# Optimization experiments

Measured on AMD Instinct MI355X. Metric: run time of the kernel, lower is better.

## Reference

```python
import jax, jax.numpy as jnp
import numpy as np

N, E, G = 30000, 60000, 1200
EMB, HID, OUT = 768, 384, 768
NEG = 0.01  # leaky_relu negative slope (torch default / GATConv negative_slope)


def _seg_softmax(a, idx, num):
    m = jax.ops.segment_max(a, idx, num_segments=num)
    e = jnp.exp(a - m[idx])
    s = jax.ops.segment_sum(e, idx, num_segments=num)
    return e / (s[idx] + 1e-16)


def _gru(x, h, Wi, Wh, bi, bh):
    gi = x @ Wi + bi
    gh = h @ Wh + bh
    ir, iz, in_ = jnp.split(gi, 3, -1)
    hr, hz, hn = jnp.split(gh, 3, -1)
    r = jax.nn.sigmoid(ir + hr)
    z = jax.nn.sigmoid(iz + hz)
    n = jnp.tanh(in_ + r * hn)
    return (1.0 - z) * n + z * h


def setup_inputs() -> dict:
    key = jax.random.key(0)
    ks = iter(jax.random.split(key, 64))
    def W(*shape):
        return jax.random.normal(next(ks), shape, jnp.float32) / np.sqrt(shape[0])
    z = lambda *s: jnp.zeros(s, jnp.float32)
    inp = {}
    inp['x_idx'] = jax.random.randint(next(ks), (N, 9), 0, 178)
    inp['edge_index'] = jax.random.randint(next(ks), (2, E), 0, N)
    inp['edge_attr_idx'] = jax.random.randint(next(ks), (E, 3), 0, 18)
    inp['batch'] = jnp.sort(jax.random.randint(next(ks), (N,), 0, G))
    inp['x_emb'] = W(178, EMB)
    inp['e_emb'] = W(18, EMB)
    inp['lin1_W'] = W(EMB, HID); inp['lin1_b'] = z(HID)
    inp['att_l'] = W(HID); inp['att_r'] = W(HID)
    inp['gl1_W'] = W(HID + EMB, HID); inp['gl2_W'] = W(HID, HID); inp['gate_b'] = z(HID)
    inp['gru1_Wi'] = W(HID, 3 * HID); inp['gru1_Wh'] = W(HID, 3 * HID)
    inp['gru1_bi'] = z(3 * HID); inp['gru1_bh'] = z(3 * HID)
    inp['gat_W'] = W(HID, HID); inp['gat_as'] = W(HID); inp['gat_ad'] = W(HID); inp['gat_b'] = z(HID)
    inp['gru2_Wi'] = W(HID, 3 * HID); inp['gru2_Wh'] = W(HID, 3 * HID)
    inp['gru2_bi'] = z(3 * HID); inp['gru2_bh'] = z(3 * HID)
    inp['mol_W'] = W(HID, HID); inp['mol_as'] = W(HID); inp['mol_ad'] = W(HID); inp['mol_b'] = z(HID)
    inp['mgru_Wi'] = W(HID, 3 * HID); inp['mgru_Wh'] = W(HID, 3 * HID)
    inp['mgru_bi'] = z(3 * HID); inp['mgru_bh'] = z(3 * HID)
    inp['lin2_W'] = W(HID, OUT); inp['lin2_b'] = z(OUT)
    return inp


def reference(x_idx, edge_index, edge_attr_idx, batch,
              x_emb, e_emb, lin1_W, lin1_b,
              att_l, att_r, gl1_W, gl2_W, gate_b,
              gru1_Wi, gru1_Wh, gru1_bi, gru1_bh,
              gat_W, gat_as, gat_ad, gat_b,
              gru2_Wi, gru2_Wh, gru2_bi, gru2_bh,
              mol_W, mol_as, mol_ad, mol_b,
              mgru_Wi, mgru_Wh, mgru_bi, mgru_bh,
              lin2_W, lin2_b):
    src, dst = edge_index[0], edge_index[1]
    # embedding-sum over feature columns
    x = x_emb[x_idx].sum(1)            # [N, EMB]
    ea = e_emb[edge_attr_idx].sum(1)   # [E, EMB]
    x = jax.nn.leaky_relu(x @ lin1_W + lin1_b, NEG)  # [N, HID]
    # --- GATEConv (edge-attr attention) ---
    m = jax.nn.leaky_relu(jnp.concatenate([x[src], ea], -1) @ gl1_W, NEG)  # [E, HID]
    a = jax.nn.leaky_relu(m @ att_l + x[dst] @ att_r, NEG)
    a = _seg_softmax(a, dst, N)
    h = jax.ops.segment_sum((m @ gl2_W) * a[:, None], dst, num_segments=N) + gate_b
    x = jax.nn.relu(_gru(jax.nn.elu(h), x, gru1_Wi, gru1_Wh, gru1_bi, gru1_bh))
    # --- atom GATConv (num_layers=2 -> one extra layer, heads=1, no self-loops) ---
    xl = x @ gat_W
    a = jax.nn.leaky_relu((xl @ gat_as)[src] + (xl @ gat_ad)[dst], NEG)
    a = _seg_softmax(a, dst, N)
    h = jax.ops.segment_sum(xl[src] * a[:, None], dst, num_segments=N) + gat_b
    x = jax.nn.relu(_gru(jax.nn.elu(h), x, gru2_Wi, gru2_Wh, gru2_bi, gru2_bh))
    # --- attentive molecule readout, num_timesteps=3 ---
    out = jax.nn.relu(jax.ops.segment_sum(x, batch, num_segments=G))  # [G, HID]
    xl = x @ mol_W
    a_node = xl @ mol_as  # per-node source attention term (fixed across timesteps)
    for _ in range(3):
        a_g = (out @ mol_W) @ mol_ad
        a = jax.nn.leaky_relu(a_node + a_g[batch], NEG)
        a = _seg_softmax(a, batch, G)
        h = jax.ops.segment_sum(xl * a[:, None], batch, num_segments=G) + mol_b
        out = jax.nn.relu(_gru(jax.nn.elu(h), out, mgru_Wi, mgru_Wh, mgru_bi, mgru_bh))
    return out @ lin2_W + lin2_b  # [G, OUT]
```

## Files before the change

### kernel.cpp

```cpp
#include <hip/hip_runtime.h>
#include <cstdint>
#include <cstddef>

#define NN 30000
#define NE 60000
#define NG 1200
#define HID 384
#define EMB 768
#define OUTD 768
#define NEGS 0.01f

typedef _Float16 f16;
typedef _Float16 f16x8 __attribute__((ext_vector_type(8)));
typedef float f32x16 __attribute__((ext_vector_type(16)));

static __device__ __forceinline__ float leaky(float x){ return x > 0.f ? x : NEGS * x; }
static __device__ __forceinline__ float elu1(float x){ return x > 0.f ? x : (expf(x) - 1.f); }
static __device__ __forceinline__ float sigm(float x){ return 1.f / (1.f + expf(-x)); }

static __device__ __forceinline__ void atomicMaxF(float* a, float v){
  if (v >= 0.f) atomicMax((int*)a, __float_as_int(v));
  else atomicMin((unsigned int*)a, __float_as_uint(v));
}

static __device__ __forceinline__ size_t pf_idx(int row, int col){
  return (((((size_t)(row >> 5)) * 24 + (col >> 4)) * 2 + ((col >> 3) & 1)) * 32
          + (row & 31)) * 8 + (col & 7);
}
#define PF_RB_STRIDE 12288
#define PF_KS_STRIDE 512
#define PF_GATE_STRIDE 147456

__global__ __launch_bounds__(256) void k_gemm(
    const float* __restrict__ A, const float* __restrict__ B,
    const float* __restrict__ bias, float* __restrict__ C,
    int M, int N, int K, int act)
{
  __shared__ float As[16][65];
  __shared__ float Bs[16][65];
  const int tid = threadIdx.x;
  const int tx = tid & 15, ty = tid >> 4;
  const int row0 = blockIdx.y * 64, col0 = blockIdx.x * 64;
  const int ar = tid >> 2, ak = (tid & 3) << 2;
  const int bk = tid >> 4, bc = (tid & 15) << 2;
  float acc[4][4] = {};
  for (int k0 = 0; k0 < K; k0 += 16) {
    float4 av = make_float4(0.f, 0.f, 0.f, 0.f);
    if (row0 + ar < M)
      av = *(const float4*)(A + (size_t)(row0 + ar) * K + k0 + ak);
    As[ak + 0][ar] = av.x; As[ak + 1][ar] = av.y;
    As[ak + 2][ar] = av.z; As[ak + 3][ar] = av.w;
    float4 bv = *(const float4*)(B + (size_t)(k0 + bk) * N + col0 + bc);
    Bs[bk][bc + 0] = bv.x; Bs[bk][bc + 1] = bv.y;
    Bs[bk][bc + 2] = bv.z; Bs[bk][bc + 3] = bv.w;
    __syncthreads();
#pragma unroll
    for (int kk = 0; kk < 16; kk++) {
      float a[4], b[4];
#pragma unroll
      for (int i = 0; i < 4; i++) a[i] = As[kk][(ty << 2) + i];
#pragma unroll
      for (int j = 0; j < 4; j++) b[j] = Bs[kk][(tx << 2) + j];
#pragma unroll
      for (int i = 0; i < 4; i++)
#pragma unroll
        for (int j = 0; j < 4; j++)
          acc[i][j] = fmaf(a[i], b[j], acc[i][j]);
    }
    __syncthreads();
  }
#pragma unroll
  for (int i = 0; i < 4; i++) {
    int r = row0 + (ty << 2) + i;
    if (r >= M) continue;
#pragma unroll
    for (int j = 0; j < 4; j++) {
      int c = col0 + (tx << 2) + j;
      float v = acc[i][j];
      if (bias) v += bias[c];
      if (act == 1) v = leaky(v);
      else if (act == 2) v = elu1(v);
      else if (act == 3) v = fmaxf(v, 0.f);
      C[(size_t)r * N + c] = v;
    }
  }
}

__global__ __launch_bounds__(256) void k_hgemm(
    const f16* __restrict__ Apf, const f16* __restrict__ Bpf,
    const float* __restrict__ bias, float* __restrict__ Cf, f16* __restrict__ Ch,
    int M, int Nn, int act)
{
  const int nct = Nn >> 7;
  const int id = blockIdx.x;
  const int lane8 = id & 7, chunk = id >> 3;
  const int ct = chunk % nct, rg = chunk / nct;
  const int rt = rg * 8 + lane8;
  const int Mt = (M + 127) >> 7;
  if (rt >= Mt) return;
  const int r0 = rt * 128, n0 = ct * 128;
  const int tid = threadIdx.x;
  const int wid = tid >> 6, lane = tid & 63;
  const int wr = wid >> 1, wc = wid & 1;
  const int l31 = lane & 31, lhi = lane >> 5;
  const size_t lane_off = (size_t)(lhi * 32 + l31) * 8;
  const f16* pA[2]; const f16* pB[2];
#pragma unroll
  for (int i = 0; i < 2; i++) {
    pA[i] = Apf + (size_t)(r0 / 32 + wr * 2 + i) * PF_RB_STRIDE + lane_off;
    pB[i] = Bpf + (size_t)(n0 / 32 + wc * 2 + i) * PF_RB_STRIDE + lane_off;
  }
  f32x16 acc[2][2];
#pragma unroll
  for (int i = 0; i < 2; i++)
#pragma unroll
    for (int j = 0; j < 2; j++)
#pragma unroll
      for (int r = 0; r < 16; r++) acc[i][j][r] = 0.f;
  f16x8 af[2], bf[2], naf[2], nbf[2];
#pragma unroll
  for (int i = 0; i < 2; i++) { af[i] = *(const f16x8*)(pA[i]); bf[i] = *(const f16x8*)(pB[i]); }
#pragma unroll 4
  for (int ks = 0; ks < 24; ks++) {
    const size_t noff = (size_t)(ks < 23 ? ks + 1 : 23) * PF_KS_STRIDE;
#pragma unroll
    for (int i = 0; i < 2; i++) { naf[i] = *(const f16x8*)(pA[i] + noff); nbf[i] = *(const f16x8*)(pB[i] + noff); }
#pragma unroll
    for (int i = 0; i < 2; i++)
#pragma unroll
      for (int j = 0; j < 2; j++)
        acc[i][j] = __builtin_amdgcn_mfma_f32_32x32x16_f16(af[i], bf[j], acc[i][j], 0, 0, 0);
#pragma unroll
    for (int i = 0; i < 2; i++) { af[i] = naf[i]; bf[i] = nbf[i]; }
  }
#pragma unroll
  for (int i = 0; i < 2; i++)
#pragma unroll
    for (int j = 0; j < 2; j++) {
      int col = n0 + wc * 64 + j * 32 + l31;
      float bv = bias ? bias[col] : 0.f;
#pragma unroll
      for (int r = 0; r < 16; r++) {
        int row = r0 + wr * 64 + i * 32 + (r & 3) + 8 * (r >> 2) + 4 * lhi;
        if (row < M) {
          float v = acc[i][j][r] + bv;
          if (act == 1) v = leaky(v);
          else if (act == 2) v = elu1(v);
          else if (act == 3) v = fmaxf(v, 0.f);
          if (Cf) Cf[(size_t)row * Nn + col] = v;
          if (Ch) Ch[pf_idx(row, col)] = (f16)v;
        }
      }
    }
}

__global__ __launch_bounds__(256) void k_gru_hgemm(
    const f16* __restrict__ Upf, const f16* __restrict__ Hpf,
    const f16* __restrict__ Wip, const f16* __restrict__ Whp,
    const float* __restrict__ bi, const float* __restrict__ bh,
    float* __restrict__ Xo, f16* __restrict__ Xoh, int M)
{
  const int id = blockIdx.x;
  const int lane8 = id & 7, chunk = id >> 3;
  const int ct = chunk % 6, rg = chunk / 6;
  const int rt = rg * 8 + lane8;
  const int Mt = (M + 63) >> 6;
  if (rt >= Mt) return;
  const int r0 = rt * 64, c0 = ct * 64;
  const int tid = threadIdx.x;
  const int wid = tid >> 6, lane = tid & 63;
  const int wr = wid >> 1, wc = wid & 1;
  const int l31 = lane & 31, lhi = lane >> 5;
  const size_t lane_off = (size_t)(lhi * 32 + l31) * 8;
  const f16* pU  = Upf + (size_t)(r0 / 32 + wr) * PF_RB_STRIDE + lane_off;
  const f16* pH  = Hpf + (size_t)(r0 / 32 + wr) * PF_RB_STRIDE + lane_off;
  const f16* pWi = Wip + (size_t)(c0 / 32 + wc) * PF_RB_STRIDE + lane_off;
  const f16* pWh = Whp + (size_t)(c0 / 32 + wc) * PF_RB_STRIDE + lane_off;
#define Z16 {0,0,0,0,0,0,0,0,0,0,0,0,0,0,0,0}
  f32x16 accR = Z16, accZ = Z16, aN = Z16, hN = Z16;
  f16x8 au, ah, bir, biz, bin, bhr, bhz, bhn;
  f16x8 nau, nah, nbir, nbiz, nbin, nbhr, nbhz, nbhn;
  au  = *(const f16x8*)(pU);
  ah  = *(const f16x8*)(pH);
  bir = *(const f16x8*)(pWi);
  biz = *(const f16x8*)(pWi + PF_GATE_STRIDE);
  bin = *(const f16x8*)(pWi + 2 * PF_GATE_STRIDE);
  bhr = *(const f16x8*)(pWh);
  bhz = *(const f16x8*)(pWh + PF_GATE_STRIDE);
  bhn = *(const f16x8*)(pWh + 2 * PF_GATE_STRIDE);
#pragma unroll 4
  for (int ks = 0; ks < 24; ks++) {
    const size_t noff = (size_t)(ks < 23 ? ks + 1 : 23) * PF_KS_STRIDE;
    nau  = *(const f16x8*)(pU + noff);
    nah  = *(const f16x8*)(pH + noff);
    nbir = *(const f16x8*)(pWi + noff);
    nbiz = *(const f16x8*)(pWi + PF_GATE_STRIDE + noff);
    nbin = *(const f16x8*)(pWi + 2 * PF_GATE_STRIDE + noff);
    nbhr = *(const f16x8*)(pWh + noff);
    nbhz = *(const f16x8*)(pWh + PF_GATE_STRIDE + noff);
    nbhn = *(const f16x8*)(pWh + 2 * PF_GATE_STRIDE + noff);
    accR = __builtin_amdgcn_mfma_f32_32x32x16_f16(au, bir, accR, 0, 0, 0);
    accR = __builtin_amdgcn_mfma_f32_32x32x16_f16(ah, bhr, accR, 0, 0, 0);
    accZ = __builtin_amdgcn_mfma_f32_32x32x16_f16(au, biz, accZ, 0, 0, 0);
    accZ = __builtin_amdgcn_mfma_f32_32x32x16_f16(ah, bhz, accZ, 0, 0, 0);
    aN   = __builtin_amdgcn_mfma_f32_32x32x16_f16(au, bin, aN, 0, 0, 0);
    hN   = __builtin_amdgcn_mfma_f32_32x32x16_f16(ah, bhn, hN, 0, 0, 0);
    au = nau; ah = nah; bir = nbir; biz = nbiz; bin = nbin;
    bhr = nbhr; bhz = nbhz; bhn = nbhn;
  }
  const int col = c0 + wc * 32 + l31;
  const float brz = bi[col] + bh[col];
  const float bzz = bi[HID + col] + bh[HID + col];
  const float bin_ = bi[2 * HID + col];
  const float bhn_ = bh[2 * HID + col];
#pragma unroll
  for (int r = 0; r < 16; r++) {
    int row = r0 + wr * 32 + (r & 3) + 8 * (r >> 2) + 4 * lhi;
    if (row < M) {
      float rg_ = sigm(accR[r] + brz);
      float zg  = sigm(accZ[r] + bzz);
      float ng  = tanhf(aN[r] + bin_ + rg_ * (hN[r] + bhn_));
      float hp  = (float)Hpf[pf_idx(row, col)];
      float o = (1.f - zg) * ng + zg * hp;
      o = fmaxf(o, 0.f);
      if (Xo) Xo[(size_t)row * HID + col] = o;
      Xoh[pf_idx(row, col)] = (f16)o;
    }
  }
}

__global__ void k_wpack_all(
    const float* __restrict__ w0, const float* __restrict__ w1,
    const float* __restrict__ w2, const float* __restrict__ w3,
    const float* __restrict__ w4, const float* __restrict__ w5,
    const float* __restrict__ w6, const float* __restrict__ w7,
    const float* __restrict__ w8, const float* __restrict__ w9,
    const float* __restrict__ w10,
    f16* __restrict__ d0, f16* __restrict__ d1, f16* __restrict__ d2,
    f16* __restrict__ d3, f16* __restrict__ d4, f16* __restrict__ d5,
    f16* __restrict__ d6, f16* __restrict__ d7, f16* __restrict__ d8,
    f16* __restrict__ d9, f16* __restrict__ d10)
{
  long t = (long)blockIdx.x * blockDim.x + threadIdx.x;
  if (t >= 3538944L) return;
  const float* W; f16* Wp; int Nn; long tt;
  if (t < 589824L) {
    int s = (int)(t / 147456L); tt = t - (long)s * 147456L; Nn = HID;
    if (s == 0) { W = w0; Wp = d0; } else if (s == 1) { W = w1; Wp = d1; }
    else if (s == 2) { W = w2; Wp = d2; } else { W = w3; Wp = d3; }
  } else if (t < 3244032L) {
    long u = t - 589824L;
    int s = (int)(u / 442368L); tt = u - (long)s * 442368L; Nn = 3 * HID;
    if (s == 0) { W = w4; Wp = d4; } else if (s == 1) { W = w5; Wp = d5; }
    else if (s == 2) { W = w6; Wp = d6; } else if (s == 3) { W = w7; Wp = d7; }
    else if (s == 4) { W = w8; Wp = d8; } else { W = w9; Wp = d9; }
  } else {
    tt = t - 3244032L; Nn = OUTD; W = w10; Wp = d10;
  }
  int elem = (int)(tt & 7); long c = tt >> 3;
  int l31 = (int)(c & 31); long q = c >> 5;
  int lhi = (int)(q & 1); long p = q >> 1;
  int ks = (int)(p % 24); int rb = (int)(p / 24);
  int n = rb * 32 + l31, k = ks * 16 + lhi * 8 + elem;
  Wp[tt] = (f16)W[(size_t)k * Nn + n];
}

__global__ void k_f2h_pf(const float* __restrict__ in, f16* __restrict__ out, long total)
{
  long t = (long)blockIdx.x * blockDim.x + threadIdx.x;
  if (t >= total) return;
  int i = (int)(t / HID), c = (int)(t % HID);
  out[pf_idx(i, c)] = (f16)in[t];
}

__global__ void k_node_embed2(const int* __restrict__ xi, const float* __restrict__ T1,
                              const float* __restrict__ b, const float* __restrict__ att_r,
                              f16* __restrict__ x1h, float* __restrict__ xr, int n)
{
  int w = (int)(((long)blockIdx.x * blockDim.x + threadIdx.x) >> 6);
  int lane = threadIdx.x & 63;
  if (w >= n) return;
  int idx[9];
#pragma unroll
  for (int j = 0; j < 9; j++) idx[j] = xi[w * 9 + j];
  float s = 0.f;
#pragma unroll
  for (int t = 0; t < 6; t++) {
    int c = lane + 64 * t;
    float v = b[c];
#pragma unroll
    for (int j = 0; j < 9; j++) v += T1[(size_t)idx[j] * HID + c];
    v = leaky(v);
    x1h[pf_idx(w, c)] = (f16)v;
    s += v * att_r[c];
  }
  for (int o = 32; o; o >>= 1) s += __shfl_down(s, o, 64);
  if (lane == 0) xr[w] = s;
}

__global__ void k_rowdot(const float* __restrict__ X, const float* __restrict__ v,
                         float* __restrict__ out, int M)
{
  int w = (int)(((long)blockIdx.x * blockDim.x + threadIdx.x) >> 6);
  int lane = threadIdx.x & 63;
  if (w >= M) return;
  float s = 0.f;
  for (int j = lane; j < HID; j += 64) s += X[(size_t)w * HID + j] * v[j];
  for (int o = 32; o; o >>= 1) s += __shfl_down(s, o, 64);
  if (lane == 0) out[w] = s;
}

__global__ void k_rowdot2(const float* __restrict__ X, const float* __restrict__ v1,
                          const float* __restrict__ v2, float* __restrict__ o1,
                          float* __restrict__ o2, int M)
{
  int w = (int)(((long)blockIdx.x * blockDim.x + threadIdx.x) >> 6);
  int lane = threadIdx.x & 63;
  if (w >= M) return;
  float s1 = 0.f, s2 = 0.f;
  for (int j = lane; j < HID; j += 64) {
    float x = X[(size_t)w * HID + j];
    s1 += x * v1[j]; s2 += x * v2[j];
  }
  for (int o = 32; o; o >>= 1) { s1 += __shfl_down(s1, o, 64); s2 += __shfl_down(s2, o, 64); }
  if (lane == 0) { o1[w] = s1; o2[w] = s2; }
}

__global__ void k_init_ms(float* __restrict__ mx, float* __restrict__ sum, int n)
{
  int t = (int)((long)blockIdx.x * blockDim.x + threadIdx.x);
  if (t >= n) return;
  mx[t] = __int_as_float(0xFF800000);
  sum[t] = 0.f;
}

__global__ void k_gbounds(const int* __restrict__ batch, int* __restrict__ gstart, int n, int G)
{
  int g = (int)((long)blockIdx.x * blockDim.x + threadIdx.x);
  if (g > G) return;
  int lo = 0, hi = n;
  while (lo < hi) { int mid = (lo + hi) >> 1; if (batch[mid] < g) lo = mid + 1; else hi = mid; }
  gstart[g] = lo;
}

__global__ __launch_bounds__(384) void k_mol_iter(
    const float* __restrict__ cur, const float* __restrict__ XLm,
    const float* __restrict__ a_node, const float* __restrict__ w_g,
    const float* __restrict__ mol_b, const int* __restrict__ gstart,
    f16* __restrict__ HMp)
{
  const int g = blockIdx.x;
  const int tid = threadIdx.x;
  const int lane = tid & 63, wv = tid >> 6;
  __shared__ float red[6];
  __shared__ float wbuf[384];
  __shared__ float sh[3];
  const int s0 = gstart[g], s1 = gstart[g + 1];
  float p = cur[(size_t)g * HID + tid] * w_g[tid];
  for (int o = 32; o; o >>= 1) p += __shfl_down(p, o, 64);
  if (lane == 0) red[wv] = p;
  __syncthreads();
  if (tid == 0) { float s = 0.f; for (int i = 0; i < 6; i++) s += red[i]; sh[0] = s; }
  __syncthreads();
  const float ag = sh[0];
  float mx = -3.4e38f;
  for (int n = s0 + tid; n < s1; n += 384) mx = fmaxf(mx, leaky(a_node[n] + ag));
  for (int o = 32; o; o >>= 1) mx = fmaxf(mx, __shfl_down(mx, o, 64));
  __syncthreads();
  if (lane == 0) red[wv] = mx;
  __syncthreads();
  if (tid == 0) { float m = red[0]; for (int i = 1; i < 6; i++) m = fmaxf(m, red[i]); sh[1] = m; }
  __syncthreads();
  const float gmx = sh[1];
  float sm = 0.f;
  for (int n = s0 + tid; n < s1; n += 384) sm += expf(leaky(a_node[n] + ag) - gmx);
  for (int o = 32; o; o >>= 1) sm += __shfl_down(sm, o, 64);
  __syncthreads();
  if (lane == 0) red[wv] = sm;
  __syncthreads();
  if (tid == 0) { float s = 0.f; for (int i = 0; i < 6; i++) s += red[i]; sh[2] = s; }
  __syncthreads();
  const float inv = 1.f / (sh[2] + 1e-16f);
  float h = 0.f;
  for (int base = s0; base < s1; base += 384) {
    int cnt = min(384, s1 - base);
    __syncthreads();
    if (tid < cnt) wbuf[tid] = expf(leaky(a_node[base + tid] + ag) - gmx) * inv;
    __syncthreads();
    for (int k = 0; k < cnt; k++) h += XLm[(size_t)(base + k) * HID + tid] * wbuf[k];
  }
  h = elu1(h + mol_b[tid]);
  HMp[pf_idx(g, tid)] = (f16)h;
}

__global__ void k_gate_att(const float* __restrict__ P, const float* __restrict__ Te,
                           const int* __restrict__ ei, const int* __restrict__ eai,
                           const float* __restrict__ attl, const float* __restrict__ xr,
                           float* __restrict__ aE, float* __restrict__ mx, int ne)
{
  int e = (int)(((long)blockIdx.x * blockDim.x + threadIdx.x) >> 6);
  int lane = threadIdx.x & 63;
  if (e >= ne) return;
  int s = ei[e];
  int i0 = eai[e * 3], i1 = eai[e * 3 + 1], i2 = eai[e * 3 + 2];
  float acc = 0.f;
  for (int j = lane; j < HID; j += 64) {
    float m = P[(size_t)s * HID + j] + Te[(size_t)i0 * HID + j]
            + Te[(size_t)i1 * HID + j] + Te[(size_t)i2 * HID + j];
    acc += leaky(m) * attl[j];
  }
  for (int o = 32; o; o >>= 1) acc += __shfl_down(acc, o, 64);
  if (lane == 0) {
    int d = ei[NE + e];
    float a = leaky(acc + xr[d]);
    aE[e] = a;
    atomicMaxF(&mx[d], a);
  }
}

__global__ void k_gat_att(const float* __restrict__ sS, const float* __restrict__ sD,
                          const int* __restrict__ ei, float* __restrict__ aE,
                          float* __restrict__ mx, int ne)
{
  int e = (int)((long)blockIdx.x * blockDim.x + threadIdx.x);
  if (e >= ne) return;
  int s = ei[e], d = ei[NE + e];
  float a = leaky(sS[s] + sD[d]);
  aE[e] = a;
  atomicMaxF(&mx[d], a);
}

__global__ void k_seg_exp(float* __restrict__ a, const int* __restrict__ idx,
                          const float* __restrict__ mx, float* __restrict__ sum, int n)
{
  int t = (int)((long)blockIdx.x * blockDim.x + threadIdx.x);
  if (t >= n) return;
  int d = idx[t];
  float e = expf(a[t] - mx[d]);
  a[t] = e;
  atomicAdd(&sum[d], e);
}

__global__ void k_scatter_edge(const float* __restrict__ P, const float* __restrict__ Te,
                               const int* __restrict__ ei, const int* __restrict__ eai,
                               const float* __restrict__ aE, const float* __restrict__ sum,
                               float* __restrict__ acc, long total)
{
  long t = (long)blockIdx.x * blockDim.x + threadIdx.x;
  if (t >= total) return;
  int e = (int)(t / HID), c = (int)(t % HID);
  int s = ei[e], d = ei[NE + e];
  float m = P[(size_t)s * HID + c] + Te[(size_t)eai[e * 3] * HID + c]
          + Te[(size_t)eai[e * 3 + 1] * HID + c] + Te[(size_t)eai[e * 3 + 2] * HID + c];
  m = leaky(m);
  float w = aE[e] / (sum[d] + 1e-16f);
  atomicAdd(&acc[(size_t)d * HID + c], m * w);
}

__global__ void k_scatter_gat(const float* __restrict__ XL, const float* __restrict__ aE,
                              const float* __restrict__ sum, const int* __restrict__ ei,
                              float* __restrict__ acc, long total)
{
  long t = (long)blockIdx.x * blockDim.x + threadIdx.x;
  if (t >= total) return;
  int e = (int)(t / HID), c = (int)(t % HID);
  int s = ei[e], d = ei[NE + e];
  float w = aE[e] / (sum[d] + 1e-16f);
  atomicAdd(&acc[(size_t)d * HID + c], XL[(size_t)s * HID + c] * w);
}

__global__ void k_scatter_sum_pf(const f16* __restrict__ Xpf, const int* __restrict__ batch,
                                 float* __restrict__ acc, long total)
{
  long t = (long)blockIdx.x * blockDim.x + threadIdx.x;
  if (t >= total) return;
  int i = (int)(t / HID), c = (int)(t % HID);
  atomicAdd(&acc[(size_t)batch[i] * HID + c], (float)Xpf[pf_idx(i, c)]);
}

__global__ void k_bias_act(float* __restrict__ X, const float* __restrict__ bias,
                           f16* __restrict__ Xh, long total, int act)
{
  long t = (long)blockIdx.x * blockDim.x + threadIdx.x;
  if (t >= total) return;
  int i = (int)(t / HID), c = (int)(t % HID);
  float v = X[t];
  if (bias) v += bias[c];
  if (act == 2) v = elu1(v);
  else if (act == 3) v = fmaxf(v, 0.f);
  X[t] = v;
  if (Xh) Xh[pf_idx(i, c)] = (f16)v;
}

extern "C" void kernel_launch(void* const* d_in, const int* in_sizes, int n_in,
                              void* d_out, int out_size, void* d_ws, size_t ws_size,
                              hipStream_t stream)
{
  const int* x_idx = (const int*)d_in[0];
  const int* edge_index = (const int*)d_in[1];
  const int* eai = (const int*)d_in[2];
  const int* batch = (const int*)d_in[3];
  const float* x_emb = (const float*)d_in[4];
  const float* e_emb = (const float*)d_in[5];
  const float* lin1_W = (const float*)d_in[6];
  const float* lin1_b = (const float*)d_in[7];
  const float* att_l = (const float*)d_in[8];
  const float* att_r = (const float*)d_in[9];
  const float* gl1_W = (const float*)d_in[10];
  const float* gl2_W = (const float*)d_in[11];
  const float* gate_b = (const float*)d_in[12];
  const float* gru1_Wi = (const float*)d_in[13];
  const float* gru1_Wh = (const float*)d_in[14];
  const float* gru1_bi = (const float*)d_in[15];
  const float* gru1_bh = (const float*)d_in[16];
  const float* gat_W = (const float*)d_in[17];
  const float* gat_as = (const float*)d_in[18];
  const float* gat_ad = (const float*)d_in[19];
  const float* gat_b = (const float*)d_in[20];
  const float* gru2_Wi = (const float*)d_in[21];
  const float* gru2_Wh = (const float*)d_in[22];
  const float* gru2_bi = (const float*)d_in[23];
  const float* gru2_bh = (const float*)d_in[24];
  const float* mol_W = (const float*)d_in[25];
  const float* mol_as = (const float*)d_in[26];
  const float* mol_ad = (const float*)d_in[27];
  const float* mol_b = (const float*)d_in[28];
  const float* mgru_Wi = (const float*)d_in[29];
  const float* mgru_Wh = (const float*)d_in[30];
  const float* mgru_bi = (const float*)d_in[31];
  const float* mgru_bh = (const float*)d_in[32];
  const float* lin2_W = (const float*)d_in[33];
  const float* lin2_b = (const float*)d_in[34];
  float* outp = (float*)d_out;

  const size_t NB = (size_t)NN * HID;
  const size_t GB = (size_t)NG * HID;
  const size_t PFH = (size_t)940 * PF_RB_STRIDE;
  const size_t PFG = (size_t)40 * PF_RB_STRIDE;

  float* ws = (float*)d_ws;
  size_t off = 0;
  auto alloc = [&](size_t n) { float* p = ws + off; off += n; return p; };
  auto alloch = [&](size_t n) { f16* p = (f16*)(ws + off); off += (n + 1) / 2; return p; };
  float* A    = alloc(NB);
  float* B    = alloc(NB);
  float* C    = alloc(NB);
  f16* H1 = alloch(PFH);
  f16* H2 = alloch(PFH);
  f16* H3 = alloch(PFH);
  f16* W1p   = alloch((size_t)HID * HID);
  f16* W2p   = alloch((size_t)HID * HID);
  f16* Wgatp = alloch((size_t)HID * HID);
  f16* Wmolp = alloch((size_t)HID * HID);
  f16* Wg1ip = alloch((size_t)3 * HID * HID);
  f16* Wg1hp = alloch((size_t)3 * HID * HID);
  f16* Wg2ip = alloch((size_t)3 * HID * HID);
  f16* Wg2hp = alloch((size_t)3 * HID * HID);
  f16* Wmgip = alloch((size_t)3 * HID * HID);
  f16* Wmghp = alloch((size_t)3 * HID * HID);
  f16* Wl2p  = alloch((size_t)HID * OUTD);
  f16* OUTaPF = alloch(PFG);
  f16* OUTbPF = alloch(PFG);
  f16* HMp    = alloch(PFG);
  float* T1   = alloc((size_t)178 * HID);
  float* Te   = alloc((size_t)18 * HID);
  float* w_g  = alloc(HID);
  float* xr   = alloc(NN);
  float* sS   = alloc(NN);
  float* sD   = alloc(NN);
  float* mxN  = alloc(NN);
  float* sumN = alloc(NN);
  float* a_node = alloc(NN);
  float* aE   = alloc(NE);
  float* OUTa = alloc(GB);
  float* OUTb = alloc(GB);
  int* gstart = (int*)alloc(NG + 1);
  (void)n_in; (void)in_sizes; (void)out_size;
  if (ws_size < off * sizeof(float)) return;

  const int* dstArr = edge_index + NE;
  dim3 blk(256);
  auto g1 = [](long n) { return dim3((unsigned)((n + 255) / 256)); };
  auto gw = [](long waves) { return dim3((unsigned)((waves * 64 + 255) / 256)); };
  const long NBt = (long)NB, EBt = (long)NE * HID, GBt = (long)GB;
  const int MtH = (NN + 127) / 128;
  const dim3 gH((unsigned)(8 * 3 * ((MtH + 7) / 8)));
  const int MtR = (NN + 63) / 64;
  const dim3 gR((unsigned)(8 * 6 * ((MtR + 7) / 8)));
  const int MtGH = (NG + 127) / 128;
  const dim3 gF((unsigned)(8 * 6 * ((MtGH + 7) / 8)));
  const int MtGR = (NG + 63) / 64;
  const dim3 gRG((unsigned)(8 * 6 * ((MtGR + 7) / 8)));

  hipLaunchKernelGGL(k_wpack_all, g1(3538944L), blk, 0, stream,
                     gl1_W, gl2_W, gat_W, mol_W,
                     gru1_Wi, gru1_Wh, gru2_Wi, gru2_Wh, mgru_Wi, mgru_Wh, lin2_W,
                     W1p, W2p, Wgatp, Wmolp,
                     Wg1ip, Wg1hp, Wg2ip, Wg2hp, Wmgip, Wmghp, Wl2p);

  hipLaunchKernelGGL(k_gemm, dim3(HID / 64, 3), blk, 0, stream,
                     x_emb, lin1_W, nullptr, T1, 178, HID, EMB, 0);
  hipLaunchKernelGGL(k_gemm, dim3(HID / 64, 1), blk, 0, stream,
                     e_emb, gl1_W + (size_t)HID * HID, nullptr, Te, 18, HID, EMB, 0);
  hipLaunchKernelGGL(k_rowdot, gw(HID), blk, 0, stream, mol_W, mol_ad, w_g, HID);
  hipLaunchKernelGGL(k_gbounds, g1(NG + 1), blk, 0, stream, batch, gstart, NN, NG);

  hipLaunchKernelGGL(k_node_embed2, gw(NN), blk, 0, stream, x_idx, T1, lin1_b, att_r, H1, xr, NN);

  hipLaunchKernelGGL(k_hgemm, gH, blk, 0, stream, H1, W1p, nullptr, B, (f16*)nullptr, NN, HID, 0);
  hipLaunchKernelGGL(k_init_ms, g1(NN), blk, 0, stream, mxN, sumN, NN);
  hipLaunchKernelGGL(k_gate_att, gw(NE), blk, 0, stream, B, Te, edge_index, eai, att_l, xr, aE, mxN, NE);
  hipLaunchKernelGGL(k_seg_exp, g1(NE), blk, 0, stream, aE, dstArr, mxN, sumN, NE);
  hipMemsetAsync(C, 0, NB * sizeof(float), stream);
  hipLaunchKernelGGL(k_scatter_edge, g1(EBt), blk, 0, stream, B, Te, edge_index, eai, aE, sumN, C, EBt);
  hipLaunchKernelGGL(k_f2h_pf, g1(NBt), blk, 0, stream, C, H2, NBt);
  hipLaunchKernelGGL(k_hgemm, gH, blk, 0, stream, H2, W2p, gate_b, (float*)nullptr, H3, NN, HID, 2);
  hipLaunchKernelGGL(k_gru_hgemm, gR, blk, 0, stream, H3, H1, Wg1ip, Wg1hp,
                     gru1_bi, gru1_bh, (float*)nullptr, H2, NN);

  hipLaunchKernelGGL(k_hgemm, gH, blk, 0, stream, H2, Wgatp, nullptr, B, (f16*)nullptr, NN, HID, 0);
  hipLaunchKernelGGL(k_rowdot2, gw(NN), blk, 0, stream, B, gat_as, gat_ad, sS, sD, NN);
  hipLaunchKernelGGL(k_init_ms, g1(NN), blk, 0, stream, mxN, sumN, NN);
  hipLaunchKernelGGL(k_gat_att, g1(NE), blk, 0, stream, sS, sD, edge_index, aE, mxN, NE);
  hipLaunchKernelGGL(k_seg_exp, g1(NE), blk, 0, stream, aE, dstArr, mxN, sumN, NE);
  hipMemsetAsync(A, 0, NB * sizeof(float), stream);
  hipLaunchKernelGGL(k_scatter_gat, g1(EBt), blk, 0, stream, B, aE, sumN, edge_index, A, EBt);
  hipLaunchKernelGGL(k_bias_act, g1(NBt), blk, 0, stream, A, gat_b, H1, NBt, 2);
  hipLaunchKernelGGL(k_gru_hgemm, gR, blk, 0, stream, H1, H2, Wg2ip, Wg2hp,
                     gru2_bi, gru2_bh, (float*)nullptr, H3, NN);

  hipMemsetAsync(OUTa, 0, GB * sizeof(float), stream);
  hipLaunchKernelGGL(k_scatter_sum_pf, g1(NBt), blk, 0, stream, H3, batch, OUTa, NBt);
  hipLaunchKernelGGL(k_bias_act, g1(GBt), blk, 0, stream, OUTa, (const float*)nullptr, OUTaPF, GBt, 3);
  hipLaunchKernelGGL(k_hgemm, gH, blk, 0, stream, H3, Wmolp, nullptr, A, (f16*)nullptr, NN, HID, 0);
  hipLaunchKernelGGL(k_rowdot, gw(NN), blk, 0, stream, A, mol_as, a_node, NN);

  float* cur = OUTa;   f16* curPF = OUTaPF;
  float* nxt = OUTb;   f16* nxtPF = OUTbPF;
  for (int t = 0; t < 3; t++) {
    hipLaunchKernelGGL(k_mol_iter, dim3(NG), dim3(384), 0, stream,
                       cur, A, a_node, w_g, mol_b, gstart, HMp);
    hipLaunchKernelGGL(k_gru_hgemm, gRG, blk, 0, stream, HMp, curPF, Wmgip, Wmghp,
                       mgru_bi, mgru_bh, nxt, nxtPF, NG);
    float* tf = cur; cur = nxt; nxt = tf;
    f16* th = curPF; curPF = nxtPF; nxtPF = th;
  }

  hipLaunchKernelGGL(k_hgemm, gF, blk, 0, stream, curPF, Wl2p, lin2_b, outp, (f16*)nullptr, NG, OUTD, 0);
}
```

Baseline: 964.2 us.

## Replace atomic edge scatter with CSR-by-destination online-softmax gather aggregation

Builds a CSR edge list grouped by destination (degree count, single-block scan, fill) and replaces the separate attention, segment max, exp-sum and per-element atomic scatter kernels with one wave per node that computes an online softmax and accumulates messages in registers. The GAT layer gets the same treatment, fusing bias and ELU into the f16 packed output. The molecule sum switches from atomic scatter to a contiguous per-graph reduction over the fp32 GRU output. This removes large float atomic traffic, several memsets and conversion passes, at the cost of CSR-build kernels and possible imbalance on high-degree nodes.

Measured after the change: 795.2 us. -17.5%, faster.

```diff
diff --git a/kernel.cpp b/kernel.cpp
--- a/kernel.cpp
+++ b/kernel.cpp
@@ -17,11 +17,6 @@
 static __device__ __forceinline__ float leaky(float x){ return x > 0.f ? x : NEGS * x; }
 static __device__ __forceinline__ float elu1(float x){ return x > 0.f ? x : (expf(x) - 1.f); }
 static __device__ __forceinline__ float sigm(float x){ return 1.f / (1.f + expf(-x)); }
-
-static __device__ __forceinline__ void atomicMaxF(float* a, float v){
-  if (v >= 0.f) atomicMax((int*)a, __float_as_int(v));
-  else atomicMin((unsigned int*)a, __float_as_uint(v));
-}
 
 static __device__ __forceinline__ size_t pf_idx(int row, int col){
   return (((((size_t)(row >> 5)) * 24 + (col >> 4)) * 2 + ((col >> 3) & 1)) * 32
@@ -265,14 +260,6 @@
   Wp[tt] = (f16)W[(size_t)k * Nn + n];
 }
 
-__global__ void k_f2h_pf(const float* __restrict__ in, f16* __restrict__ out, long total)
-{
-  long t = (long)blockIdx.x * blockDim.x + threadIdx.x;
-  if (t >= total) return;
-  int i = (int)(t / HID), c = (int)(t % HID);
-  out[pf_idx(i, c)] = (f16)in[t];
-}
-
 __global__ void k_node_embed2(const int* __restrict__ xi, const float* __restrict__ T1,
                               const float* __restrict__ b, const float* __restrict__ att_r,
                               f16* __restrict__ x1h, float* __restrict__ xr, int n)
@@ -326,14 +313,6 @@
   if (lane == 0) { o1[w] = s1; o2[w] = s2; }
 }
 
-__global__ void k_init_ms(float* __restrict__ mx, float* __restrict__ sum, int n)
-{
-  int t = (int)((long)blockIdx.x * blockDim.x + threadIdx.x);
-  if (t >= n) return;
-  mx[t] = __int_as_float(0xFF800000);
-  sum[t] = 0.f;
-}
-
 __global__ void k_gbounds(const int* __restrict__ batch, int* __restrict__ gstart, int n, int G)
 {
   int g = (int)((long)blockIdx.x * blockDim.x + threadIdx.x);
@@ -341,6 +320,150 @@
   int lo = 0, hi = n;
   while (lo < hi) { int mid = (lo + hi) >> 1; if (batch[mid] < g) lo = mid + 1; else hi = mid; }
   gstart[g] = lo;
+}
+
+__global__ void k_deg(const int* __restrict__ dst, int* __restrict__ cnt, int ne)
+{
+  int e = (int)((long)blockIdx.x * blockDim.x + threadIdx.x);
+  if (e >= ne) return;
+  atomicAdd(&cnt[dst[e]], 1);
+}
+
+__global__ __launch_bounds__(1024) void k_scan(const int* __restrict__ cnt,
+                                               int* __restrict__ rowptr,
+                                               int* __restrict__ cursor)
+{
+  __shared__ int part[1024];
+  const int tid = threadIdx.x;
+  const int c0 = tid * 30, c1 = min(c0 + 30, NN);
+  int s = 0;
+  for (int i = c0; i < c1; i++) s += cnt[i];
+  part[tid] = s;
+  __syncthreads();
+  for (int o = 1; o < 1024; o <<= 1) {
+    int v = (tid >= o) ? part[tid - o] : 0;
+    __syncthreads();
+    part[tid] += v;
+    __syncthreads();
+  }
+  int run = (tid ? part[tid - 1] : 0);
+  for (int i = c0; i < c1; i++) { rowptr[i] = run; cursor[i] = run; run += cnt[i]; }
+  if (tid == 1023) rowptr[NN] = part[1023];
+}
+
+__global__ void k_fill(const int* __restrict__ dst, int* __restrict__ cursor,
+                       int* __restrict__ elist, int ne)
+{
+  int e = (int)((long)blockIdx.x * blockDim.x + threadIdx.x);
+  if (e >= ne) return;
+  int p = atomicAdd(&cursor[dst[e]], 1);
+  elist[p] = e;
+}
+
+__global__ void k_gate_agg(const float* __restrict__ P, const float* __restrict__ Te,
+                           const int* __restrict__ ei, const int* __restrict__ eai,
+                           const float* __restrict__ attl, const float* __restrict__ xr,
+                           const int* __restrict__ rowptr, const int* __restrict__ elist,
+                           f16* __restrict__ Hout, int n)
+{
+  int node = (int)(((long)blockIdx.x * blockDim.x + threadIdx.x) >> 6);
+  int lane = threadIdx.x & 63;
+  if (node >= n) return;
+  const int e0 = rowptr[node], e1 = rowptr[node + 1];
+  const float xrd = xr[node];
+  float h0 = 0.f, h1 = 0.f, h2 = 0.f, h3 = 0.f, h4 = 0.f, h5 = 0.f;
+  float mx = -3.4e38f, s = 0.f;
+  for (int q = e0; q < e1; q++) {
+    int e = elist[q];
+    int src = ei[e];
+    int i0 = eai[e * 3], i1 = eai[e * 3 + 1], i2 = eai[e * 3 + 2];
+    float m[6];
+    float dot = 0.f;
+#pragma unroll
+    for (int t = 0; t < 6; t++) {
+      int c = lane + 64 * t;
+      float v = P[(size_t)src * HID + c] + Te[(size_t)i0 * HID + c]
+              + Te[(size_t)i1 * HID + c] + Te[(size_t)i2 * HID + c];
+      v = leaky(v);
+      m[t] = v;
+      dot += v * attl[c];
+    }
+#pragma unroll
+    for (int o = 32; o; o >>= 1) dot += __shfl_xor(dot, o, 64);
+    float a = leaky(dot + xrd);
+    if (a > mx) {
+      float f = expf(mx - a);
+      s *= f; h0 *= f; h1 *= f; h2 *= f; h3 *= f; h4 *= f; h5 *= f;
+      mx = a;
+    }
+    float w = expf(a - mx);
+    s += w;
+    h0 += w * m[0]; h1 += w * m[1]; h2 += w * m[2];
+    h3 += w * m[3]; h4 += w * m[4]; h5 += w * m[5];
+  }
+  const float inv = 1.f / (s + 1e-16f);
+  Hout[pf_idx(node, lane)]           = (f16)(h0 * inv);
+  Hout[pf_idx(node, lane + 64)]      = (f16)(h1 * inv);
+  Hout[pf_idx(node, lane + 128)]     = (f16)(h2 * inv);
+  Hout[pf_idx(node, lane + 192)]     = (f16)(h3 * inv);
+  Hout[pf_idx(node, lane + 256)]     = (f16)(h4 * inv);
+  Hout[pf_idx(node, lane + 320)]     = (f16)(h5 * inv);
+}
+
+__global__ void k_gat_agg(const float* __restrict__ XL, const int* __restrict__ ei,
+                          const float* __restrict__ sS, const float* __restrict__ sD,
+                          const float* __restrict__ gat_b,
+                          const int* __restrict__ rowptr, const int* __restrict__ elist,
+                          f16* __restrict__ Hout, int n)
+{
+  int node = (int)(((long)blockIdx.x * blockDim.x + threadIdx.x) >> 6);
+  int lane = threadIdx.x & 63;
+  if (node >= n) return;
+  const int e0 = rowptr[node], e1 = rowptr[node + 1];
+  const float sDn = sD[node];
+  float h0 = 0.f, h1 = 0.f, h2 = 0.f, h3 = 0.f, h4 = 0.f, h5 = 0.f;
+  float mx = -3.4e38f, s = 0.f;
+  for (int q = e0; q < e1; q++) {
+    int e = elist[q];
+    int src = ei[e];
+    float a = leaky(sS[src] + sDn);
+    if (a > mx) {
+      float f = expf(mx - a);
+      s *= f; h0 *= f; h1 *= f; h2 *= f; h3 *= f; h4 *= f; h5 *= f;
+      mx = a;
+    }
+    float w = expf(a - mx);
+    s += w;
+    const float* row = XL + (size_t)src * HID;
+    h0 += w * row[lane];
+    h1 += w * row[lane + 64];
+    h2 += w * row[lane + 128];
+    h3 += w * row[lane + 192];
+    h4 += w * row[lane + 256];
+    h5 += w * row[lane + 320];
+  }
+  const float inv = 1.f / (s + 1e-16f);
+  Hout[pf_idx(node, lane)]       = (f16)elu1(h0 * inv + gat_b[lane]);
+  Hout[pf_idx(node, lane + 64)]  = (f16)elu1(h1 * inv + gat_b[lane + 64]);
+  Hout[pf_idx(node, lane + 128)] = (f16)elu1(h2 * inv + gat_b[lane + 128]);
+  Hout[pf_idx(node, lane + 192)] = (f16)elu1(h3 * inv + gat_b[lane + 192]);
+  Hout[pf_idx(node, lane + 256)] = (f16)elu1(h4 * inv + gat_b[lane + 256]);
+  Hout[pf_idx(node, lane + 320)] = (f16)elu1(h5 * inv + gat_b[lane + 320]);
+}
+
+__global__ __launch_bounds__(384) void k_graph_sum(const float* __restrict__ X,
+                                                   const int* __restrict__ gstart,
+                                                   float* __restrict__ OUTa,
+                                                   f16* __restrict__ OUTaPF)
+{
+  const int g = blockIdx.x;
+  const int tid = threadIdx.x;
+  const int s0 = gstart[g], s1 = gstart[g + 1];
+  float acc = 0.f;
+  for (int i = s0; i < s1; i++) acc += X[(size_t)i * HID + tid];
+  acc = fmaxf(acc, 0.f);
+  OUTa[(size_t)g * HID + tid] = acc;
+  OUTaPF[pf_idx(g, tid)] = (f16)acc;
 }
 
 __global__ __launch_bounds__(384) void k_mol_iter(
@@ -391,105 +514,6 @@
   }
   h = elu1(h + mol_b[tid]);
   HMp[pf_idx(g, tid)] = (f16)h;
-}
-
-__global__ void k_gate_att(const float* __restrict__ P, const float* __restrict__ Te,
-                           const int* __restrict__ ei, const int* __restrict__ eai,
-                           const float* __restrict__ attl, const float* __restrict__ xr,
-                           float* __restrict__ aE, float* __restrict__ mx, int ne)
-{
-  int e = (int)(((long)blockIdx.x * blockDim.x + threadIdx.x) >> 6);
-  int lane = threadIdx.x & 63;
-  if (e >= ne) return;
-  int s = ei[e];
-  int i0 = eai[e * 3], i1 = eai[e * 3 + 1], i2 = eai[e * 3 + 2];
-  float acc = 0.f;
-  for (int j = lane; j < HID; j += 64) {
-    float m = P[(size_t)s * HID + j] + Te[(size_t)i0 * HID + j]
-            + Te[(size_t)i1 * HID + j] + Te[(size_t)i2 * HID + j];
-    acc += leaky(m) * attl[j];
-  }
-  for (int o = 32; o; o >>= 1) acc += __shfl_down(acc, o, 64);
-  if (lane == 0) {
-    int d = ei[NE + e];
-    float a = leaky(acc + xr[d]);
-    aE[e] = a;
-    atomicMaxF(&mx[d], a);
-  }
-}
-
-__global__ void k_gat_att(const float* __restrict__ sS, const float* __restrict__ sD,
-                          const int* __restrict__ ei, float* __restrict__ aE,
-                          float* __restrict__ mx, int ne)
-{
-  int e = (int)((long)blockIdx.x * blockDim.x + threadIdx.x);
-  if (e >= ne) return;
-  int s = ei[e], d = ei[NE + e];
-  float a = leaky(sS[s] + sD[d]);
-  aE[e] = a;
-  atomicMaxF(&mx[d], a);
-}
-
-__global__ void k_seg_exp(float* __restrict__ a, const int* __restrict__ idx,
-                          const float* __restrict__ mx, float* __restrict__ sum, int n)
-{
-  int t = (int)((long)blockIdx.x * blockDim.x + threadIdx.x);
-  if (t >= n) return;
-  int d = idx[t];
-  float e = expf(a[t] - mx[d]);
-  a[t] = e;
-  atomicAdd(&sum[d], e);
-}
-
-__global__ void k_scatter_edge(const float* __restrict__ P, const float* __restrict__ Te,
-                               const int* __restrict__ ei, const int* __restrict__ eai,
-                               const float* __restrict__ aE, const float* __restrict__ sum,
-                               float* __restrict__ acc, long total)
-{
-  long t = (long)blockIdx.x * blockDim.x + threadIdx.x;
-  if (t >= total) return;
-  int e = (int)(t / HID), c = (int)(t % HID);
-  int s = ei[e], d = ei[NE + e];
-  float m = P[(size_t)s * HID + c] + Te[(size_t)eai[e * 3] * HID + c]
-          + Te[(size_t)eai[e * 3 + 1] * HID + c] + Te[(size_t)eai[e * 3 + 2] * HID + c];
-  m = leaky(m);
-  float w = aE[e] / (sum[d] + 1e-16f);
-  atomicAdd(&acc[(size_t)d * HID + c], m * w);
-}
-
-__global__ void k_scatter_gat(const float* __restrict__ XL, const float* __restrict__ aE,
-                              const float* __restrict__ sum, const int* __restrict__ ei,
-                              float* __restrict__ acc, long total)
-{
-  long t = (long)blockIdx.x * blockDim.x + threadIdx.x;
-  if (t >= total) return;
-  int e = (int)(t / HID), c = (int)(t % HID);
-  int s = ei[e], d = ei[NE + e];
-  float w = aE[e] / (sum[d] + 1e-16f);
-  atomicAdd(&acc[(size_t)d * HID + c], XL[(size_t)s * HID + c] * w);
-}
-
-__global__ void k_scatter_sum_pf(const f16* __restrict__ Xpf, const int* __restrict__ batch,
-                                 float* __restrict__ acc, long total)
-{
-  long t = (long)blockIdx.x * blockDim.x + threadIdx.x;
-  if (t >= total) return;
-  int i = (int)(t / HID), c = (int)(t % HID);
-  atomicAdd(&acc[(size_t)batch[i] * HID + c], (float)Xpf[pf_idx(i, c)]);
-}
-
-__global__ void k_bias_act(float* __restrict__ X, const float* __restrict__ bias,
-                           f16* __restrict__ Xh, long total, int act)
-{
-  long t = (long)blockIdx.x * blockDim.x + threadIdx.x;
-  if (t >= total) return;
-  int i = (int)(t / HID), c = (int)(t % HID);
-  float v = X[t];
-  if (bias) v += bias[c];
-  if (act == 2) v = elu1(v);
-  else if (act == 3) v = fmaxf(v, 0.f);
-  X[t] = v;
-  if (Xh) Xh[pf_idx(i, c)] = (f16)v;
 }
 
 extern "C" void kernel_launch(void* const* d_in, const int* in_sizes, int n_in,
@@ -544,7 +568,6 @@
   auto alloch = [&](size_t n) { f16* p = (f16*)(ws + off); off += (n + 1) / 2; return p; };
   float* A    = alloc(NB);
   float* B    = alloc(NB);
-  float* C    = alloc(NB);
   f16* H1 = alloch(PFH);
   f16* H2 = alloch(PFH);
   f16* H3 = alloch(PFH);
@@ -568,13 +591,14 @@
   float* xr   = alloc(NN);
   float* sS   = alloc(NN);
   float* sD   = alloc(NN);
-  float* mxN  = alloc(NN);
-  float* sumN = alloc(NN);
   float* a_node = alloc(NN);
-  float* aE   = alloc(NE);
   float* OUTa = alloc(GB);
   float* OUTb = alloc(GB);
-  int* gstart = (int*)alloc(NG + 1);
+  int* gstart = (int*)alloc(NG + 2);
+  int* cnt    = (int*)alloc(NN);
+  int* rowptr = (int*)alloc(NN + 2);
+  int* cursor = (int*)alloc(NN);
+  int* elist  = (int*)alloc(NE);
   (void)n_in; (void)in_sizes; (void)out_size;
   if (ws_size < off * sizeof(float)) return;
 
@@ -582,7 +606,6 @@
   dim3 blk(256);
   auto g1 = [](long n) { return dim3((unsigned)((n + 255) / 256)); };
   auto gw = [](long waves) { return dim3((unsigned)((waves * 64 + 255) / 256)); };
-  const long NBt = (long)NB, EBt = (long)NE * HID, GBt = (long)GB;
   const int MtH = (NN + 127) / 128;
   const dim3 gH((unsigned)(8 * 3 * ((MtH + 7) / 8)));
   const int MtR = (NN + 63) / 64;
@@ -597,41 +620,34 @@
                      gru1_Wi, gru1_Wh, gru2_Wi, gru2_Wh, mgru_Wi, mgru_Wh, lin2_W,
                      W1p, W2p, Wgatp, Wmolp,
                      Wg1ip, Wg1hp, Wg2ip, Wg2hp, Wmgip, Wmghp, Wl2p);
-
   hipLaunchKernelGGL(k_gemm, dim3(HID / 64, 3), blk, 0, stream,
                      x_emb, lin1_W, nullptr, T1, 178, HID, EMB, 0);
   hipLaunchKernelGGL(k_gemm, dim3(HID / 64, 1), blk, 0, stream,
                      e_emb, gl1_W + (size_t)HID * HID, nullptr, Te, 18, HID, EMB, 0);
   hipLaunchKernelGGL(k_rowdot, gw(HID), blk, 0, stream, mol_W, mol_ad, w_g, HID);
   hipLaunchKernelGGL(k_gbounds, g1(NG + 1), blk, 0, stream, batch, gstart, NN, NG);
+  hipMemsetAsync(cnt, 0, NN * sizeof(int), stream);
+  hipLaunchKernelGGL(k_deg, g1(NE), blk, 0, stream, dstArr, cnt, NE);
+  hipLaunchKernelGGL(k_scan, dim3(1), dim3(1024), 0, stream, cnt, rowptr, cursor);
+  hipLaunchKernelGGL(k_fill, g1(NE), blk, 0, stream, dstArr, cursor, elist, NE);
 
   hipLaunchKernelGGL(k_node_embed2, gw(NN), blk, 0, stream, x_idx, T1, lin1_b, att_r, H1, xr, NN);
 
   hipLaunchKernelGGL(k_hgemm, gH, blk, 0, stream, H1, W1p, nullptr, B, (f16*)nullptr, NN, HID, 0);
-  hipLaunchKernelGGL(k_init_ms, g1(NN), blk, 0, stream, mxN, sumN, NN);
-  hipLaunchKernelGGL(k_gate_att, gw(NE), blk, 0, stream, B, Te, edge_index, eai, att_l, xr, aE, mxN, NE);
-  hipLaunchKernelGGL(k_seg_exp, g1(NE), blk, 0, stream, aE, dstArr, mxN, sumN, NE);
-  hipMemsetAsync(C, 0, NB * sizeof(float), stream);
-  hipLaunchKernelGGL(k_scatter_edge, g1(EBt), blk, 0, stream, B, Te, edge_index, eai, aE, sumN, C, EBt);
-  hipLaunchKernelGGL(k_f2h_pf, g1(NBt), blk, 0, stream, C, H2, NBt);
+  hipLaunchKernelGGL(k_gate_agg, gw(NN), blk, 0, stream, B, Te, edge_index, eai, att_l, xr,
+                     rowptr, elist, H2, NN);
   hipLaunchKernelGGL(k_hgemm, gH, blk, 0, stream, H2, W2p, gate_b, (float*)nullptr, H3, NN, HID, 2);
   hipLaunchKernelGGL(k_gru_hgemm, gR, blk, 0, stream, H3, H1, Wg1ip, Wg1hp,
                      gru1_bi, gru1_bh, (float*)nullptr, H2, NN);
 
   hipLaunchKernelGGL(k_hgemm, gH, blk, 0, stream, H2, Wgatp, nullptr, B, (f16*)nullptr, NN, HID, 0);
   hipLaunchKernelGGL(k_rowdot2, gw(NN), blk, 0, stream, B, gat_as, gat_ad, sS, sD, NN);
-  hipLaunchKernelGGL(k_init_ms, g1(NN), blk, 0, stream, mxN, sumN, NN);
-  hipLaunchKernelGGL(k_gat_att, g1(NE), blk, 0, stream, sS, sD, edge_index, aE, mxN, NE);
-  hipLaunchKernelGGL(k_seg_exp, g1(NE), blk, 0, stream, aE, dstArr, mxN, sumN, NE);
-  hipMemsetAsync(A, 0, NB * sizeof(float), stream);
-  hipLaunchKernelGGL(k_scatter_gat, g1(EBt), blk, 0, stream, B, aE, sumN, edge_index, A, EBt);
-  hipLaunchKernelGGL(k_bias_act, g1(NBt), blk, 0, stream, A, gat_b, H1, NBt, 2);
+  hipLaunchKernelGGL(k_gat_agg, gw(NN), blk, 0, stream, B, edge_index, sS, sD, gat_b,
+                     rowptr, elist, H1, NN);
   hipLaunchKernelGGL(k_gru_hgemm, gR, blk, 0, stream, H1, H2, Wg2ip, Wg2hp,
-                     gru2_bi, gru2_bh, (float*)nullptr, H3, NN);
-
-  hipMemsetAsync(OUTa, 0, GB * sizeof(float), stream);
-  hipLaunchKernelGGL(k_scatter_sum_pf, g1(NBt), blk, 0, stream, H3, batch, OUTa, NBt);
-  hipLaunchKernelGGL(k_bias_act, g1(GBt), blk, 0, stream, OUTa, (const float*)nullptr, OUTaPF, GBt, 3);
+                     gru2_bi, gru2_bh, B, H3, NN);
+
+  hipLaunchKernelGGL(k_graph_sum, dim3(NG), dim3(384), 0, stream, B, gstart, OUTa, OUTaPF);
   hipLaunchKernelGGL(k_hgemm, gH, blk, 0, stream, H3, Wmolp, nullptr, A, (f16*)nullptr, NN, HID, 0);
   hipLaunchKernelGGL(k_rowdot, gw(NN), blk, 0, stream, A, mol_as, a_node, NN);
 
```
